# Kernel optimization log

Measured on AMD Instinct MI355X. Metric: run time of the kernel, lower is better.

Reference implementation:

```python
import jax, jax.numpy as jnp
import numpy as np

L = 16  # block size; g = c // L; lc = c // g


def linear(x, W, b):
    # x: [..., in], W: [in, out], b: [out]
    return jnp.dot(x, W) + b


def setup_inputs() -> dict:
    key = jax.random.key(0)
    ks = jax.random.split(key, 20)
    c = 256
    L2 = L * L
    s = 0.02
    inp = {"x": jax.random.normal(ks[0], (4, 32, 32, 32, c), dtype=jnp.float32)}
    names = [("W_h", (c, c)), ("b_h", (c,)), ("W_w", (c, c)), ("b_w", (c,)),
             ("W_c", (c, c)), ("b_c", (c,)), ("W_d", (c, c)), ("b_d", (c,)),
             ("W_attn", (L2, L2)), ("b_attn", (L2,)),
             ("W_1", (c, c)), ("b_1", (c,)), ("W_2", (c, c)), ("b_2", (c,)),
             ("W_3", (c, c)), ("b_3", (c,))]
    for i, (nm, shp) in enumerate(names):
        inp[nm] = jax.random.normal(ks[i + 1], shp, dtype=jnp.float32) * s
    return inp


def ip_mlp(x, W_h, b_h, W_w, b_w, W_c, b_c, W_attn, b_attn, W_1, b_1):
    b, h, w, d, c = x.shape
    g = c // L
    lc = c // g
    h1, w1 = h // L, w // L
    # x_att: b (h1 lh) (w1 lw) d c -> b h1 w1 d c (lh lw)
    xa = x.reshape(b, h1, L, w1, L, d, c).transpose(0, 1, 3, 5, 6, 2, 4)
    xa = xa.reshape(b, h1, w1, d, c, L * L)
    xa = linear(xa, W_attn, b_attn)
    xa = xa.reshape(b, h1, w1, d, c, L, L).transpose(0, 1, 5, 2, 6, 3, 4)
    x_att = xa.reshape(b, h, w, d, c)
    # x_h: b (h1 lh) w d (lc g) -> b (h1 w) lc d (lh g)
    xh = x.reshape(b, h1, L, w, d, lc, g).transpose(0, 1, 3, 5, 4, 2, 6)
    xh = xh.reshape(b, h1 * w, lc, d, L * g)
    xh = linear(xh, W_h, b_h)
    xh = xh.reshape(b, h1, w, lc, d, L, g).transpose(0, 1, 5, 2, 4, 3, 6)
    x_h = xh.reshape(b, h, w, d, c)
    # x_w: b h (w1 lw) d (lc g) -> b (h w1) lc d (lw g)
    xw = x.reshape(b, h, w1, L, d, lc, g).transpose(0, 1, 2, 5, 4, 3, 6)
    xw = xw.reshape(b, h * w1, lc, d, L * g)
    xw = linear(xw, W_w, b_w)
    xw = xw.reshape(b, h, w1, lc, d, L, g).transpose(0, 1, 2, 5, 4, 3, 6)
    x_w = xw.reshape(b, h, w, d, c)
    x_c = linear(x, W_c, b_c)
    out = (1.0 + x_att) * (x_h + x_w + x_c)
    return linear(out, W_1, b_1)


def tp_mlp(x, W_d, b_d, W_2, b_2):
    b, h, w, d, c = x.shape
    g = c // L
    l = c // g
    d1 = d // L
    # b h w (d1 ld) (l g) -> b h w d1 l (ld g)
    xd = x.reshape(b, h, w, d1, L, l, g).transpose(0, 1, 2, 3, 5, 4, 6)
    xd = xd.reshape(b, h, w, d1, l, L * g)
    xd = linear(xd, W_d, b_d)
    xd = xd.reshape(b, h, w, d1, l, L, g).transpose(0, 1, 2, 3, 5, 4, 6)
    xd = xd.reshape(b, h, w, d, c)
    return linear(xd, W_2, b_2)


def reference(x, W_h, b_h, W_w, b_w, W_c, b_c, W_d, b_d, W_attn, b_attn,
              W_1, b_1, W_2, b_2, W_3, b_3):
    x = x + ip_mlp(x, W_h, b_h, W_w, b_w, W_c, b_c, W_attn, b_attn, W_1, b_1)
    x = x + tp_mlp(x, W_d, b_d, W_2, b_2)
    x = x + linear(x, W_3, b_3)
    return x
```

## Files before the change

### kernel.cpp

```cpp
#include <hip/hip_runtime.h>


typedef __attribute__((ext_vector_type(8))) short bf16x8;
typedef __attribute__((ext_vector_type(8))) unsigned short u16x8;
typedef __attribute__((ext_vector_type(4))) float f32x4;
typedef __attribute__((ext_vector_type(4))) unsigned short u16x4;
typedef unsigned short u16;
typedef unsigned int u32;

#define DEV __device__ __forceinline__

DEV u16 f2b(float f) {
  union { float f; u32 u; } v; v.f = f;
  u32 r = v.u + 0x7FFFu + ((v.u >> 16) & 1u);
  return (u16)(r >> 16);
}
DEV float b2f(u16 b) {
  union { u32 u; float f; } v; v.u = ((u32)b) << 16; return v.f;
}

DEV int lds_off(int row, int colByte) {
  return (row << 9) + (colByte ^ ((row & 31) << 4));
}
DEV int lds_off256(int row, int colByte) {
  return (row << 8) + (colByte ^ ((row & 15) << 4));
}
DEV bf16x8 ld_lds(const u16* lds, int row, int colByte) {
  return *(const bf16x8*)((const char*)lds + lds_off(row, colByte));
}
DEV bf16x8 ld_glb(const u16* g, int row, int kByte) {
  return *(const bf16x8*)((const char*)g + (row << 9) + kByte);
}
DEV f32x4 ldx_nt(const float* p) { return __builtin_nontemporal_load((const f32x4*)p); }
DEV void stf4_nt(float* p, f32x4 v) { __builtin_nontemporal_store(v, (f32x4*)p); }

template <int MI, int NJ>
DEV void zero_acc(f32x4 acc[MI][NJ]) {
#pragma unroll
  for (int i = 0; i < MI; ++i)
#pragma unroll
    for (int j = 0; j < NJ; ++j) {
      acc[i][j][0] = 0.f; acc[i][j][1] = 0.f; acc[i][j][2] = 0.f; acc[i][j][3] = 0.f;
    }
}

template <int MI, int NJ, typename LA, typename LB>
DEV void gemmT(LA loadA, LB loadB, f32x4 acc[MI][NJ]) {
#pragma unroll
  for (int kk = 0; kk < 8; ++kk) {
    bf16x8 a[MI], b[NJ];
#pragma unroll
    for (int i = 0; i < MI; ++i) a[i] = loadA(i, kk);
#pragma unroll
    for (int j = 0; j < NJ; ++j) b[j] = loadB(j, kk);
#pragma unroll
    for (int i = 0; i < MI; ++i)
#pragma unroll
      for (int j = 0; j < NJ; ++j)
        acc[i][j] = __builtin_amdgcn_mfma_f32_16x16x32_bf16(a[i], b[j], acc[i][j], 0, 0, 0);
  }
}

#define WAVE_SETUP                  \
  const int tid = threadIdx.x;      \
  const int lane = tid & 63;        \
  const int wave = tid >> 6;        \
  const int wm = wave >> 2;         \
  const int wn = wave & 3;          \
  const int lr = lane & 15;         \
  const int lk = lane >> 4;

__global__ void k_pack_all(const float* W0, const float* W1p, const float* W2p,
                           const float* W3p, const float* W4p, const float* W5p,
                           const float* W6p, const float* W7p, u16* __restrict__ WT) {
  int bi = blockIdx.x;
  int wsel = bi >> 8, n = bi & 255;
  const float* W;
  switch (wsel) {
    case 0: W = W0; break; case 1: W = W1p; break; case 2: W = W2p; break;
    case 3: W = W3p; break; case 4: W = W4p; break; case 5: W = W5p; break;
    case 6: W = W6p; break; default: W = W7p; break;
  }
  u16* dst = WT + wsel * 65536;
  int k0 = threadIdx.x * 4;
#pragma unroll
  for (int i = 0; i < 4; ++i) {
    int k = k0 + i;
    float v = __builtin_nontemporal_load(W + k * 256 + n);
    if (wsel == 7 && k == n) v += 1.0f;
    dst[n * 256 + k] = f2b(v);
  }
}

__global__ __launch_bounds__(512, 4) void k_att(const float* __restrict__ x,
    const u16* __restrict__ WTattn, const float* __restrict__ b_attn,
    u16* __restrict__ att, u16* __restrict__ xbf) {
  __shared__ alignas(16) u16 XT[32768];
  WAVE_SETUP;
  const int ch = blockIdx.x & 1;
  const int t = blockIdx.x >> 1;
  const int d = t & 31, w1 = (t >> 5) & 1, h1 = (t >> 6) & 1, b = t >> 7;
  const int B0 = (((b * 32 + h1 * 16) * 32 + w1 * 16) * 32 + d) * 256;

  for (int i = tid; i < 8192; i += 512) {
    int q = i >> 5;
    int c4 = (i & 31) << 2;
    const int gofs = B0 + (q >> 4) * 262144 + (q & 15) * 8192 + ch * 128 + c4;
    const f32x4 v = ldx_nt(x + gofs);
    u16x4 pk;
    pk[0] = f2b(v[0]); pk[1] = f2b(v[1]); pk[2] = f2b(v[2]); pk[3] = f2b(v[3]);
    XT[lds_off(c4 + 0, q * 2) >> 1] = pk[0];
    XT[lds_off(c4 + 1, q * 2) >> 1] = pk[1];
    XT[lds_off(c4 + 2, q * 2) >> 1] = pk[2];
    XT[lds_off(c4 + 3, q * 2) >> 1] = pk[3];
    *(u16x4*)(xbf + gofs) = pk;
  }
  __syncthreads();

  f32x4 acc[8][2];
  zero_acc<8, 2>(acc);
  gemmT<8, 2>(
      [&](int i, int kk) { return ld_glb(WTattn, wm * 128 + i * 16 + lr, kk * 64 + lk * 16); },
      [&](int j, int kk) { return ld_lds(XT, wn * 32 + j * 16 + lr, kk * 64 + lk * 16); },
      acc);

  __syncthreads();
#pragma unroll
  for (int i = 0; i < 8; ++i)
#pragma unroll
    for (int j = 0; j < 2; ++j)
#pragma unroll
      for (int r = 0; r < 4; ++r) {
        int p = wm * 128 + i * 16 + lk * 4 + r;
        int cl = wn * 32 + j * 16 + lr;
        XT[lds_off256(p, cl * 2) >> 1] = f2b(acc[i][j][r] + b_attn[p]);
      }
  __syncthreads();
  u16* out = att + t * 65536;
  for (int i = tid; i < 4096; i += 512) {
    int p = i >> 4, sB = (i & 15) << 4;
    bf16x8 v = *(const bf16x8*)((const char*)XT + p * 256 + sB);
    int c8l = (sB ^ ((p & 15) << 4)) >> 1;
    *(bf16x8*)(out + p * 256 + ch * 128 + c8l) = v;
  }
}

__global__ __launch_bounds__(512, 1) void k_hw(const u16* __restrict__ xbf,
    const u16* __restrict__ WTh, const u16* __restrict__ WTw,
    u16* __restrict__ h_out, u16* __restrict__ w_out) {
  __shared__ alignas(16) u16 XS[65536];
  __shared__ alignas(16) u16 BB[16384];
  WAVE_SETUP;
  const int t = blockIdx.x;
  const int d = t & 31, w1 = (t >> 5) & 1, h1 = (t >> 6) & 1, b = t >> 7;
  const int B0 = (((b * 32 + h1 * 16) * 32 + w1 * 16) * 32 + d) * 256;
  u16* h_t = h_out + t * 65536;
  u16* w_t = w_out + t * 65536;

  for (int i = tid; i < 8192; i += 512) {
    int pos = i >> 5, c8 = (i & 31) << 3;
    u16x8 v = *(const u16x8*)(xbf + B0 + (pos >> 4) * 262144 + (pos & 15) * 8192 + c8);
    *(u16x8*)((char*)XS + lds_off(pos, c8 * 2)) = v;
  }
  __syncthreads();

  for (int s = 0; s < 4; ++s) {
    f32x4 hacc[8][1];
    zero_acc<8, 1>(hacc);
    gemmT<8, 1>(
        [&](int i, int kk) {
          int k = kk * 32 + lk * 8;
          return *(const bf16x8*)((const char*)XS +
                                  lds_off((k >> 4) * 16 + lr, (wm * 8 + i) * 32 + (k & 15) * 2));
        },
        [&](int j, int kk) { return ld_glb(WTh, s * 64 + wn * 16 + lr, kk * 64 + lk * 16); },
        hacc);
    __syncthreads();
#pragma unroll
    for (int i = 0; i < 8; ++i)
#pragma unroll
      for (int r = 0; r < 4; ++r)
        BB[lds_off(wn * 16 + lk * 4 + r, ((wm * 8 + i) * 16 + lr) * 2) >> 1] = f2b(hacc[i][0][r]);
    __syncthreads();
    for (int i2 = tid; i2 < 2048; i2 += 512) {
      int posl = i2 >> 5, sB = (i2 & 31) << 4;
      bf16x8 v = *(const bf16x8*)((const char*)BB + posl * 512 + sB);
      int c8 = (sB ^ ((posl & 31) << 4)) >> 1;
      *(bf16x8*)(h_t + (s * 64 + posl) * 256 + c8) = v;
    }
  }

  for (int q = 0; q < 4; ++q) {
    f32x4 wacc[8][1];
    zero_acc<8, 1>(wacc);
    gemmT<8, 1>(
        [&](int i, int kk) {
          int k = kk * 32 + lk * 8;
          return *(const bf16x8*)((const char*)XS +
                                  lds_off(lr * 16 + (k >> 4), (wm * 8 + i) * 32 + (k & 15) * 2));
        },
        [&](int j, int kk) { return ld_glb(WTw, q * 64 + wn * 16 + lr, kk * 64 + lk * 16); },
        wacc);
    __syncthreads();
#pragma unroll
    for (int i = 0; i < 8; ++i)
#pragma unroll
      for (int r = 0; r < 4; ++r)
        BB[lds_off((lk * 4 + r) * 4 + wn, ((wm * 8 + i) * 16 + lr) * 2) >> 1] = f2b(wacc[i][0][r]);
    __syncthreads();
    for (int i2 = tid; i2 < 2048; i2 += 512) {
      int rb = i2 >> 5, sB = (i2 & 31) << 4;
      bf16x8 v = *(const bf16x8*)((const char*)BB + rb * 512 + sB);
      int c8 = (sB ^ ((rb & 31) << 4)) >> 1;
      int pos = (rb >> 2) * 16 + 4 * q + (rb & 3);
      *(bf16x8*)(w_t + pos * 256 + c8) = v;
    }
  }
}

__global__ __launch_bounds__(512, 2) void k_comb(const u16* __restrict__ xbf,
    const u16* __restrict__ h_out, const u16* __restrict__ w_out, const u16* __restrict__ att,
    const float* __restrict__ bh, const float* __restrict__ bw, const float* __restrict__ bc,
    const u16* __restrict__ WTc, const u16* __restrict__ WT1, const float* __restrict__ b1,
    u16* __restrict__ x1) {
  __shared__ alignas(16) u16 XS[32768];
  __shared__ alignas(16) u16 BB[32768];
  WAVE_SETUP;
  const int ph = blockIdx.x & 1;
  const int t = blockIdx.x >> 1;
  const int d = t & 31, w1 = (t >> 5) & 1, h1 = (t >> 6) & 1, b = t >> 7;
  const int B0 = (((b * 32 + h1 * 16) * 32 + w1 * 16) * 32 + d) * 256;
  const u16* h_t = h_out + t * 65536;
  const u16* w_t = w_out + t * 65536;
  const u16* att_t = att + t * 65536;

  for (int i = tid; i < 4096; i += 512) {
    int posl = i >> 5, c8 = (i & 31) << 3;
    int pos = ph * 128 + posl;
    u16x8 v = *(const u16x8*)(xbf + B0 + (pos >> 4) * 262144 + (pos & 15) * 8192 + c8);
    *(u16x8*)((char*)XS + lds_off(posl, c8 * 2)) = v;
  }
  __syncthreads();

  f32x4 acc[4][4];
  zero_acc<4, 4>(acc);
  gemmT<4, 4>(
      [&](int i, int kk) { return ld_lds(XS, wm * 64 + i * 16 + lr, kk * 64 + lk * 16); },
      [&](int j, int kk) { return ld_glb(WTc, wn * 64 + j * 16 + lr, kk * 64 + lk * 16); },
      acc);
#pragma unroll
  for (int i = 0; i < 4; ++i) {
    int lh = ph * 8 + wm * 4 + i;
#pragma unroll
    for (int j = 0; j < 4; ++j) {
      float bcv = bc[wn * 64 + j * 16 + lr];
#pragma unroll
      for (int r = 0; r < 4; ++r) {
        int posl = wm * 64 + i * 16 + lk * 4 + r;
        int n = wn * 64 + j * 16 + lr;
        float v = acc[i][j][r] + bcv + bh[lh * 16 + lr] + bw[(lk * 4 + r) * 16 + lr];
        BB[lds_off(posl, n * 2) >> 1] = f2b(v);
      }
    }
  }
  __syncthreads();

  for (int i2 = tid; i2 < 4096; i2 += 512) {
    int posl = i2 >> 5, c8 = (i2 & 31) << 3;
    int pos = ph * 128 + posl;
    u16x8 hv = *(const u16x8*)(h_t + pos * 256 + c8);
    u16x8 wv = *(const u16x8*)(w_t + pos * 256 + c8);
    u16x8 av = *(const u16x8*)(att_t + pos * 256 + c8);
    u16x8* p = (u16x8*)((char*)BB + lds_off(posl, c8 * 2));
    u16x8 cur = *p, o;
#pragma unroll
    for (int j = 0; j < 8; ++j)
      o[j] = f2b((1.0f + b2f(av[j])) * (b2f(cur[j]) + b2f(hv[j]) + b2f(wv[j])));
    *p = o;
  }
  __syncthreads();

  zero_acc<4, 4>(acc);
  gemmT<4, 4>(
      [&](int i, int kk) { return ld_lds(BB, wm * 64 + i * 16 + lr, kk * 64 + lk * 16); },
      [&](int j, int kk) { return ld_glb(WT1, wn * 64 + j * 16 + lr, kk * 64 + lk * 16); },
      acc);
  __syncthreads();
#pragma unroll
  for (int i = 0; i < 4; ++i)
#pragma unroll
    for (int j = 0; j < 4; ++j) {
      float b1v = b1[wn * 64 + j * 16 + lr];
#pragma unroll
      for (int r = 0; r < 4; ++r) {
        int posl = wm * 64 + i * 16 + lk * 4 + r;
        int n = wn * 64 + j * 16 + lr;
        BB[lds_off(posl, n * 2) >> 1] = f2b(acc[i][j][r] + b1v);
      }
    }
  __syncthreads();

  for (int i2 = tid; i2 < 4096; i2 += 512) {
    int posl = i2 >> 5, sB = (i2 & 31) << 4;
    bf16x8 v = *(const bf16x8*)((const char*)BB + posl * 512 + sB);
    bf16x8 xv = *(const bf16x8*)((const char*)XS + posl * 512 + sB);
    int c8 = (sB ^ ((posl & 31) << 4)) >> 1;
    int pos = ph * 128 + posl;
    u16x8 o;
#pragma unroll
    for (int j = 0; j < 8; ++j) o[j] = f2b(b2f((u16)v[j]) + b2f((u16)xv[j]));
    *(u16x8*)(x1 + B0 + (pos >> 4) * 262144 + (pos & 15) * 8192 + c8) = o;
  }
}

__global__ __launch_bounds__(512, 2) void k_d(const u16* __restrict__ x1,
    const u16* __restrict__ WTd, const float* __restrict__ bd, u16* __restrict__ xd) {
  __shared__ alignas(16) u16 XS[32768];
  WAVE_SETUP;
  const int bid = blockIdx.x;
  const int wh = bid & 1, d1 = (bid >> 1) & 1, wb = (bid >> 2) & 1,
            h = (bid >> 3) & 31, b = bid >> 8;
  const int W0 = (b * 32 + h) * 32 + wb * 16 + wh * 8;

  for (int i = tid; i < 4096; i += 512) {
    int Rl = i >> 5;
    int c8 = (i & 31) << 3;
    int wloLoc = Rl >> 4, ld = Rl & 15;
    const u16x8 v = *(const u16x8*)(x1 + (size_t)(W0 + wloLoc) * 8192 +
                                    (d1 * 16 + ld) * 256 + c8);
    *(u16x8*)((char*)XS + lds_off(Rl, c8 * 2)) = v;
  }
  __syncthreads();

  f32x4 acc[4][4];
  zero_acc<4, 4>(acc);
  gemmT<4, 4>(
      [&](int i, int kk) {
        int k = kk * 32 + lk * 8;
        int khi = k >> 4, kloB = (k & 15) * 2;
        int mt = wm * 4 + i;
        return *(const bf16x8*)((const char*)XS + lds_off(mt * 16 + khi, lr * 32 + kloB));
      },
      [&](int j, int kk) { return ld_glb(WTd, wn * 64 + j * 16 + lr, kk * 64 + lk * 16); },
      acc);
  __syncthreads();
#pragma unroll
  for (int i = 0; i < 4; ++i)
#pragma unroll
    for (int j = 0; j < 4; ++j)
#pragma unroll
      for (int r = 0; r < 4; ++r) {
        int mloc = wm * 64 + i * 16 + lk * 4 + r;
        int n = wn * 64 + j * 16 + lr;
        int row = ((mloc >> 4) << 4) + (n >> 4);
        int col = ((mloc & 15) << 4) + (n & 15);
        XS[lds_off(row, col * 2) >> 1] = f2b(acc[i][j][r] + bd[n]);
      }
  __syncthreads();
  const int B0d = (((b * 32 + h) * 32 + wb * 16) * 32 + d1 * 16) * 256;
  for (int i = tid; i < 4096; i += 512) {
    int Rl = i >> 5, sB = (i & 31) << 4;
    bf16x8 v = *(const bf16x8*)((const char*)XS + Rl * 512 + sB);
    int c8 = (sB ^ ((Rl & 31) << 4)) >> 1;
    *(bf16x8*)(xd + B0d + (wh * 8 + (Rl >> 4)) * 8192 + (Rl & 15) * 256 + c8) = v;
  }
}

__global__ __launch_bounds__(512, 2) void k_fin(const u16* __restrict__ x1,
    const u16* __restrict__ xd, const u16* __restrict__ WT2, const u16* __restrict__ WT3p,
    const float* __restrict__ b2, const float* __restrict__ b3, float* __restrict__ outp) {
  __shared__ alignas(16) u16 X2[32768];
  WAVE_SETUP;
  const int ph = blockIdx.x & 1;
  const int vt = blockIdx.x >> 1;
  const size_t base = (size_t)vt * 65536;

  for (int i = tid; i < 4096; i += 512) {
    int Rl = i >> 5, c8 = (i & 31) << 3;
    const u16x8 v = *(const u16x8*)(x1 + base + (size_t)(ph * 128 + Rl) * 256 + c8);
    *(u16x8*)((char*)X2 + lds_off(Rl, c8 * 2)) = v;
  }

  const u16* xd_t = xd + base;
  f32x4 acc[4][4];
  zero_acc<4, 4>(acc);
  gemmT<4, 4>(
      [&](int i, int kk) { return ld_glb(xd_t, ph * 128 + wm * 64 + i * 16 + lr, kk * 64 + lk * 16); },
      [&](int j, int kk) { return ld_glb(WT2, wn * 64 + j * 16 + lr, kk * 64 + lk * 16); },
      acc);
  __syncthreads();

#pragma unroll
  for (int i = 0; i < 4; ++i)
#pragma unroll
    for (int j = 0; j < 4; ++j)
#pragma unroll
      for (int r = 0; r < 4; ++r) {
        int mloc = wm * 64 + i * 16 + lk * 4 + r;
        int n = wn * 64 + j * 16 + lr;
        int off = lds_off(mloc, n * 2) >> 1;
        X2[off] = f2b(b2f(X2[off]) + acc[i][j][r] + b2[n]);
      }
  __syncthreads();

  zero_acc<4, 4>(acc);
  gemmT<4, 4>(
      [&](int i, int kk) { return ld_lds(X2, wm * 64 + i * 16 + lr, kk * 64 + lk * 16); },
      [&](int j, int kk) { return ld_glb(WT3p, wn * 64 + j * 16 + lr, kk * 64 + lk * 16); },
      acc);

  float* X2f = (float*)X2;
#pragma unroll
  for (int half = 0; half < 2; ++half) {
    __syncthreads();
    if (wm == half) {
#pragma unroll
      for (int i = 0; i < 4; ++i)
#pragma unroll
        for (int j = 0; j < 4; ++j)
#pragma unroll
          for (int r = 0; r < 4; ++r) {
            int row = i * 16 + lk * 4 + r;
            int n = wn * 64 + j * 16 + lr;
            X2f[row * 256 + n] = acc[i][j][r] + b3[n];
          }
    }
    __syncthreads();
    for (int i = tid; i < 4096; i += 512) {
      int row = i >> 6, c4 = (i & 63) << 2;
      f32x4 v = *(const f32x4*)(X2f + row * 256 + c4);
      stf4_nt(outp + base + (size_t)(ph * 128 + half * 64 + row) * 256 + c4, v);
    }
  }
}

extern "C" void kernel_launch(void* const* d_in, const int* in_sizes, int n_in,
                              void* d_out, int out_size, void* d_ws, size_t ws_size,
                              hipStream_t stream) {
  (void)in_sizes; (void)n_in; (void)out_size; (void)ws_size;
  const float* x      = (const float*)d_in[0];
  const float* W_h    = (const float*)d_in[1];
  const float* b_h    = (const float*)d_in[2];
  const float* W_w    = (const float*)d_in[3];
  const float* b_w    = (const float*)d_in[4];
  const float* W_c    = (const float*)d_in[5];
  const float* b_c    = (const float*)d_in[6];
  const float* W_d    = (const float*)d_in[7];
  const float* b_d    = (const float*)d_in[8];
  const float* W_attn = (const float*)d_in[9];
  const float* b_attn = (const float*)d_in[10];
  const float* W_1    = (const float*)d_in[11];
  const float* b_1    = (const float*)d_in[12];
  const float* W_2    = (const float*)d_in[13];
  const float* b_2    = (const float*)d_in[14];
  const float* W_3    = (const float*)d_in[15];
  const float* b_3    = (const float*)d_in[16];
  float* outp = (float*)d_out;

  u16* WT = (u16*)d_ws;
  u16* R1 = WT + 8 * 65536;
  u16* R2 = R1 + 33554432;
  u16* HOS = (u16*)d_out;
  u16* WOS = HOS + 33554432;

  k_pack_all<<<2048, 64, 0, stream>>>(W_h, W_w, W_c, W_attn, W_1, W_d, W_2, W_3, WT);

  k_att <<<1024, 512, 0, stream>>>(x, WT + 3 * 65536, b_attn, R2, R1);
  k_hw  <<<512, 512, 0, stream>>>(R1, WT + 0 * 65536, WT + 1 * 65536, HOS, WOS);
  k_comb<<<1024, 512, 0, stream>>>(R1, HOS, WOS, R2, b_h, b_w, b_c,
                                   WT + 2 * 65536, WT + 4 * 65536, b_1, R1);
  k_d   <<<1024, 512, 0, stream>>>(R1, WT + 5 * 65536, b_d, R2);
  k_fin <<<1024, 512, 0, stream>>>(R1, R2, WT + 6 * 65536, WT + 7 * 65536, b_2, b_3, outp);
}
```

Before: 546.8 us.

## Fuse tp_mlp depth mixing with final GEMMs into one kernel, shrink LDS

Merges k_d and k_fin into a single k_tp kernel. Each block now handles 64 rows (4 w positions by 16 depth) and chains the W_d, W_2 and W_3 GEMMs through LDS, so the intermediate xd never goes to global memory. k_comb drops its second 64 KB LDS buffer by reusing one buffer and re-reading the residual x from global, which lowers LDS use per block. The cost is smaller per-block GEMM tiles (2x4 instead of 4x4), more blocks, and more reloads of the weights from global or L2.

```diff
diff --git a/kernel.cpp b/kernel.cpp
--- a/kernel.cpp
+++ b/kernel.cpp
@@ -223,8 +223,7 @@
     const float* __restrict__ bh, const float* __restrict__ bw, const float* __restrict__ bc,
     const u16* __restrict__ WTc, const u16* __restrict__ WT1, const float* __restrict__ b1,
     u16* __restrict__ x1) {
-  __shared__ alignas(16) u16 XS[32768];
-  __shared__ alignas(16) u16 BB[32768];
+  __shared__ alignas(16) u16 T[32768];
   WAVE_SETUP;
   const int ph = blockIdx.x & 1;
   const int t = blockIdx.x >> 1;
@@ -238,16 +237,18 @@
     int posl = i >> 5, c8 = (i & 31) << 3;
     int pos = ph * 128 + posl;
     u16x8 v = *(const u16x8*)(xbf + B0 + (pos >> 4) * 262144 + (pos & 15) * 8192 + c8);
-    *(u16x8*)((char*)XS + lds_off(posl, c8 * 2)) = v;
+    *(u16x8*)((char*)T + lds_off(posl, c8 * 2)) = v;
   }
   __syncthreads();
 
   f32x4 acc[4][4];
   zero_acc<4, 4>(acc);
   gemmT<4, 4>(
-      [&](int i, int kk) { return ld_lds(XS, wm * 64 + i * 16 + lr, kk * 64 + lk * 16); },
+      [&](int i, int kk) { return ld_lds(T, wm * 64 + i * 16 + lr, kk * 64 + lk * 16); },
       [&](int j, int kk) { return ld_glb(WTc, wn * 64 + j * 16 + lr, kk * 64 + lk * 16); },
       acc);
+  __syncthreads();
+
 #pragma unroll
   for (int i = 0; i < 4; ++i) {
     int lh = ph * 8 + wm * 4 + i;
@@ -259,7 +260,7 @@
         int posl = wm * 64 + i * 16 + lk * 4 + r;
         int n = wn * 64 + j * 16 + lr;
         float v = acc[i][j][r] + bcv + bh[lh * 16 + lr] + bw[(lk * 4 + r) * 16 + lr];
-        BB[lds_off(posl, n * 2) >> 1] = f2b(v);
+        T[lds_off(posl, n * 2) >> 1] = f2b(v);
       }
     }
   }
@@ -271,7 +272,7 @@
     u16x8 hv = *(const u16x8*)(h_t + pos * 256 + c8);
     u16x8 wv = *(const u16x8*)(w_t + pos * 256 + c8);
     u16x8 av = *(const u16x8*)(att_t + pos * 256 + c8);
-    u16x8* p = (u16x8*)((char*)BB + lds_off(posl, c8 * 2));
+    u16x8* p = (u16x8*)((char*)T + lds_off(posl, c8 * 2));
     u16x8 cur = *p, o;
 #pragma unroll
     for (int j = 0; j < 8; ++j)
@@ -282,10 +283,11 @@
 
   zero_acc<4, 4>(acc);
   gemmT<4, 4>(
-      [&](int i, int kk) { return ld_lds(BB, wm * 64 + i * 16 + lr, kk * 64 + lk * 16); },
+      [&](int i, int kk) { return ld_lds(T, wm * 64 + i * 16 + lr, kk * 64 + lk * 16); },
       [&](int j, int kk) { return ld_glb(WT1, wn * 64 + j * 16 + lr, kk * 64 + lk * 16); },
       acc);
   __syncthreads();
+
 #pragma unroll
   for (int i = 0; i < 4; ++i)
 #pragma unroll
@@ -295,141 +297,119 @@
       for (int r = 0; r < 4; ++r) {
         int posl = wm * 64 + i * 16 + lk * 4 + r;
         int n = wn * 64 + j * 16 + lr;
-        BB[lds_off(posl, n * 2) >> 1] = f2b(acc[i][j][r] + b1v);
+        T[lds_off(posl, n * 2) >> 1] = f2b(acc[i][j][r] + b1v);
       }
     }
   __syncthreads();
 
   for (int i2 = tid; i2 < 4096; i2 += 512) {
     int posl = i2 >> 5, sB = (i2 & 31) << 4;
-    bf16x8 v = *(const bf16x8*)((const char*)BB + posl * 512 + sB);
-    bf16x8 xv = *(const bf16x8*)((const char*)XS + posl * 512 + sB);
+    bf16x8 v = *(const bf16x8*)((const char*)T + posl * 512 + sB);
     int c8 = (sB ^ ((posl & 31) << 4)) >> 1;
     int pos = ph * 128 + posl;
+    const int gofs = B0 + (pos >> 4) * 262144 + (pos & 15) * 8192 + c8;
+    u16x8 xv = *(const u16x8*)(xbf + gofs);
     u16x8 o;
 #pragma unroll
-    for (int j = 0; j < 8; ++j) o[j] = f2b(b2f((u16)v[j]) + b2f((u16)xv[j]));
-    *(u16x8*)(x1 + B0 + (pos >> 4) * 262144 + (pos & 15) * 8192 + c8) = o;
-  }
-}
-
-__global__ __launch_bounds__(512, 2) void k_d(const u16* __restrict__ x1,
-    const u16* __restrict__ WTd, const float* __restrict__ bd, u16* __restrict__ xd) {
-  __shared__ alignas(16) u16 XS[32768];
+    for (int j = 0; j < 8; ++j) o[j] = f2b(b2f((u16)v[j]) + b2f(xv[j]));
+    *(u16x8*)(x1 + gofs) = o;
+  }
+}
+
+__global__ __launch_bounds__(512, 2) void k_tp(const u16* __restrict__ x1,
+    const u16* __restrict__ WTd, const u16* __restrict__ WT2, const u16* __restrict__ WT3p,
+    const float* __restrict__ bd, const float* __restrict__ b2, const float* __restrict__ b3,
+    float* __restrict__ outp) {
+  __shared__ alignas(16) u16 XS[16384];
+  __shared__ alignas(16) u16 BB[16384];
   WAVE_SETUP;
   const int bid = blockIdx.x;
-  const int wh = bid & 1, d1 = (bid >> 1) & 1, wb = (bid >> 2) & 1,
-            h = (bid >> 3) & 31, b = bid >> 8;
-  const int W0 = (b * 32 + h) * 32 + wb * 16 + wh * 8;
-
-  for (int i = tid; i < 4096; i += 512) {
-    int Rl = i >> 5;
-    int c8 = (i & 31) << 3;
-    int wloLoc = Rl >> 4, ld = Rl & 15;
-    const u16x8 v = *(const u16x8*)(x1 + (size_t)(W0 + wloLoc) * 8192 +
-                                    (d1 * 16 + ld) * 256 + c8);
+  const int wg = bid & 7, d1 = (bid >> 3) & 1, h = (bid >> 4) & 31, b = bid >> 9;
+  const int W0 = (b * 32 + h) * 32 + wg * 4;
+
+  for (int i = tid; i < 2048; i += 512) {
+    int Rl = i >> 5, c8 = (i & 31) << 3;
+    const u16x8 v = *(const u16x8*)(x1 + (size_t)(W0 + (Rl >> 4)) * 8192 +
+                                    (d1 * 16 + (Rl & 15)) * 256 + c8);
     *(u16x8*)((char*)XS + lds_off(Rl, c8 * 2)) = v;
   }
   __syncthreads();
 
-  f32x4 acc[4][4];
-  zero_acc<4, 4>(acc);
-  gemmT<4, 4>(
+  f32x4 acc[2][4];
+  zero_acc<2, 4>(acc);
+  gemmT<2, 4>(
       [&](int i, int kk) {
         int k = kk * 32 + lk * 8;
-        int khi = k >> 4, kloB = (k & 15) * 2;
-        int mt = wm * 4 + i;
-        return *(const bf16x8*)((const char*)XS + lds_off(mt * 16 + khi, lr * 32 + kloB));
+        int mt = wm * 2 + i;
+        return *(const bf16x8*)((const char*)XS + lds_off(mt * 16 + (k >> 4),
+                                                          lr * 32 + (k & 15) * 2));
       },
       [&](int j, int kk) { return ld_glb(WTd, wn * 64 + j * 16 + lr, kk * 64 + lk * 16); },
       acc);
-  __syncthreads();
-#pragma unroll
-  for (int i = 0; i < 4; ++i)
+#pragma unroll
+  for (int i = 0; i < 2; ++i)
 #pragma unroll
     for (int j = 0; j < 4; ++j)
 #pragma unroll
       for (int r = 0; r < 4; ++r) {
-        int mloc = wm * 64 + i * 16 + lk * 4 + r;
+        int mloc = wm * 32 + i * 16 + lk * 4 + r;
         int n = wn * 64 + j * 16 + lr;
         int row = ((mloc >> 4) << 4) + (n >> 4);
         int col = ((mloc & 15) << 4) + (n & 15);
-        XS[lds_off(row, col * 2) >> 1] = f2b(acc[i][j][r] + bd[n]);
+        BB[lds_off(row, col * 2) >> 1] = f2b(acc[i][j][r] + bd[n]);
       }
   __syncthreads();
-  const int B0d = (((b * 32 + h) * 32 + wb * 16) * 32 + d1 * 16) * 256;
-  for (int i = tid; i < 4096; i += 512) {
-    int Rl = i >> 5, sB = (i & 31) << 4;
-    bf16x8 v = *(const bf16x8*)((const char*)XS + Rl * 512 + sB);
-    int c8 = (sB ^ ((Rl & 31) << 4)) >> 1;
-    *(bf16x8*)(xd + B0d + (wh * 8 + (Rl >> 4)) * 8192 + (Rl & 15) * 256 + c8) = v;
-  }
-}
-
-__global__ __launch_bounds__(512, 2) void k_fin(const u16* __restrict__ x1,
-    const u16* __restrict__ xd, const u16* __restrict__ WT2, const u16* __restrict__ WT3p,
-    const float* __restrict__ b2, const float* __restrict__ b3, float* __restrict__ outp) {
-  __shared__ alignas(16) u16 X2[32768];
-  WAVE_SETUP;
-  const int ph = blockIdx.x & 1;
-  const int vt = blockIdx.x >> 1;
-  const size_t base = (size_t)vt * 65536;
-
-  for (int i = tid; i < 4096; i += 512) {
-    int Rl = i >> 5, c8 = (i & 31) << 3;
-    const u16x8 v = *(const u16x8*)(x1 + base + (size_t)(ph * 128 + Rl) * 256 + c8);
-    *(u16x8*)((char*)X2 + lds_off(Rl, c8 * 2)) = v;
-  }
-
-  const u16* xd_t = xd + base;
-  f32x4 acc[4][4];
-  zero_acc<4, 4>(acc);
-  gemmT<4, 4>(
-      [&](int i, int kk) { return ld_glb(xd_t, ph * 128 + wm * 64 + i * 16 + lr, kk * 64 + lk * 16); },
+
+  zero_acc<2, 4>(acc);
+  gemmT<2, 4>(
+      [&](int i, int kk) { return ld_lds(BB, (wm * 2 + i) * 16 + lr, kk * 64 + lk * 16); },
       [&](int j, int kk) { return ld_glb(WT2, wn * 64 + j * 16 + lr, kk * 64 + lk * 16); },
       acc);
   __syncthreads();
 
 #pragma unroll
-  for (int i = 0; i < 4; ++i)
-#pragma unroll
-    for (int j = 0; j < 4; ++j)
+  for (int i = 0; i < 2; ++i)
+#pragma unroll
+    for (int j = 0; j < 4; ++j) {
+      float b2v = b2[wn * 64 + j * 16 + lr];
 #pragma unroll
       for (int r = 0; r < 4; ++r) {
-        int mloc = wm * 64 + i * 16 + lk * 4 + r;
+        int mloc = wm * 32 + i * 16 + lk * 4 + r;
         int n = wn * 64 + j * 16 + lr;
         int off = lds_off(mloc, n * 2) >> 1;
-        X2[off] = f2b(b2f(X2[off]) + acc[i][j][r] + b2[n]);
+        BB[off] = f2b(b2f(XS[off]) + acc[i][j][r] + b2v);
       }
-  __syncthreads();
-
-  zero_acc<4, 4>(acc);
-  gemmT<4, 4>(
-      [&](int i, int kk) { return ld_lds(X2, wm * 64 + i * 16 + lr, kk * 64 + lk * 16); },
+    }
+  __syncthreads();
+
+  zero_acc<2, 4>(acc);
+  gemmT<2, 4>(
+      [&](int i, int kk) { return ld_lds(BB, (wm * 2 + i) * 16 + lr, kk * 64 + lk * 16); },
       [&](int j, int kk) { return ld_glb(WT3p, wn * 64 + j * 16 + lr, kk * 64 + lk * 16); },
       acc);
 
-  float* X2f = (float*)X2;
+  float* XSf = (float*)XS;
 #pragma unroll
   for (int half = 0; half < 2; ++half) {
     __syncthreads();
     if (wm == half) {
 #pragma unroll
-      for (int i = 0; i < 4; ++i)
+      for (int i = 0; i < 2; ++i)
 #pragma unroll
         for (int j = 0; j < 4; ++j)
 #pragma unroll
           for (int r = 0; r < 4; ++r) {
             int row = i * 16 + lk * 4 + r;
             int n = wn * 64 + j * 16 + lr;
-            X2f[row * 256 + n] = acc[i][j][r] + b3[n];
+            XSf[row * 256 + n] = acc[i][j][r] + b3[n];
           }
     }
     __syncthreads();
-    for (int i = tid; i < 4096; i += 512) {
-      int row = i >> 6, c4 = (i & 63) << 2;
-      f32x4 v = *(const f32x4*)(X2f + row * 256 + c4);
-      stf4_nt(outp + base + (size_t)(ph * 128 + half * 64 + row) * 256 + c4, v);
+    for (int i2 = tid; i2 < 2048; i2 += 512) {
+      int row = i2 >> 6, c4 = (i2 & 63) << 2;
+      int Rg = half * 32 + row;
+      f32x4 v = *(const f32x4*)(XSf + row * 256 + c4);
+      stf4_nt(outp + (size_t)(W0 + (Rg >> 4)) * 8192 + (d1 * 16 + (Rg & 15)) * 256 + c4, v);
     }
   }
 }
@@ -469,6 +449,6 @@
   k_hw  <<<512, 512, 0, stream>>>(R1, WT + 0 * 65536, WT + 1 * 65536, HOS, WOS);
   k_comb<<<1024, 512, 0, stream>>>(R1, HOS, WOS, R2, b_h, b_w, b_c,
                                    WT + 2 * 65536, WT + 4 * 65536, b_1, R1);
-  k_d   <<<1024, 512, 0, stream>>>(R1, WT + 5 * 65536, b_d, R2);
-  k_fin <<<1024, 512, 0, stream>>>(R1, R2, WT + 6 * 65536, WT + 7 * 65536, b_2, b_3, outp);
-}
+  k_tp  <<<2048, 512, 0, stream>>>(R1, WT + 5 * 65536, WT + 6 * 65536, WT + 7 * 65536,
+                                   b_d, b_2, b_3, outp);
+}
```

After: 552.0 us. About the same (+0.9%).
